# Kernel tuning notes

Hardware: AMD Instinct MI355X
Metric: run time of the kernel (lower is better)

## Reference

```python
import jax, jax.numpy as jnp
import numpy as np

PC_RANGE = np.array([-20.0, -20.0, -2.3, 20.0, 20.0, 0.9], np.float32)
GRID = np.array([0.1, 0.1, 0.1], np.float32)
K = 5                      # kernel_size
C_IN, C_OUT = 128, 128
BS, G = 8, 2000
SPATIAL = tuple(int(s) for s in ((PC_RANGE[3:] - PC_RANGE[:3]) / GRID).astype(np.int32))  # (400,400,32)


def setup_inputs() -> dict:
    key = jax.random.key(0)
    k1, k2, k3 = jax.random.split(key, 3)
    instance_feature = jax.random.normal(k1, (BS, G, C_IN), jnp.float32)
    anchor = jax.random.uniform(k2, (BS, G, 3), jnp.float32)          # normalized xyz in [0,1)
    w = jax.random.normal(k3, (K ** 3, C_IN, C_OUT), jnp.float32) * 0.02  # SubMConv3d weight, flattened offsets
    return {"instance_feature": instance_feature, "anchor": anchor, "w": w}


def _voxel_indices(anchor):
    # cartesian(): map normalized anchor xyz into the pc_range box, then voxelize.
    lo = jnp.asarray(PC_RANGE[:3])
    hi = jnp.asarray(PC_RANGE[3:])
    xyz = anchor[..., :3] * (hi - lo) + lo                 # [bs, g, 3]
    idx = ((xyz - lo) / jnp.asarray(GRID)).astype(jnp.int32)
    return idx


def reference(instance_feature, anchor, w):
    bs, g, c = instance_feature.shape
    n = bs * g
    idx = _voxel_indices(anchor).reshape(n, 3)             # [n, 3] int32 voxel coords
    bidx = jnp.repeat(jnp.arange(bs, dtype=jnp.int32), g)  # [n]
    Dx, Dy, Dz = SPATIAL

    # Rulebook substitute: dense voxel -> point-id lookup (-1 = inactive).
    grid = jnp.full((bs, Dx, Dy, Dz), -1, jnp.int32)
    grid = grid.at[bidx, idx[:, 0], idx[:, 1], idx[:, 2]].set(jnp.arange(n, dtype=jnp.int32))

    feats = instance_feature.reshape(n, c)
    r = (K - 1) // 2
    ax = jnp.arange(-r, r + 1, dtype=jnp.int32)
    offs = jnp.stack(jnp.meshgrid(ax, ax, ax, indexing="ij"), -1).reshape(-1, 3)  # [K^3, 3]
    dims = jnp.asarray([Dx, Dy, Dz], jnp.int32)

    # Submanifold conv: gather neighbor features per kernel offset, matmul, accumulate.
    def step(acc, inp):
        off, wk = inp                                       # off [3], wk [Cin, Cout]
        nb = idx + off[None, :]                             # [n, 3]
        inb = jnp.all((nb >= 0) & (nb < dims[None, :]), axis=-1)
        nbc = jnp.clip(nb, 0, dims[None, :] - 1)
        j = grid[bidx, nbc[:, 0], nbc[:, 1], nbc[:, 2]]     # [n] neighbor point id or -1
        valid = inb & (j >= 0)
        fj = jnp.where(valid[:, None], feats[jnp.clip(j, 0, n - 1)], 0.0)  # [n, Cin]
        return acc + fj @ wk, None

    out0 = jnp.zeros((n, C_OUT), feats.dtype)
    out, _ = jax.lax.scan(step, out0, (offs, w))
    return out.reshape(bs, g, C_OUT)                        # output_proj = Identity
```

## Files before the change

kernel.cpp:

```cpp
#include <hip/hip_runtime.h>
#include <stdint.h>

#define BSZ 8
#define GQ 2000
#define NPTS (BSZ * GQ)
#define CH 128
#define TM 16
#define NTHR 256
#define AS_LD 129
#define KB 32
#define ZPAD 32
#define EMPTY16 0xAAAAu
#define BHCAP 64
#define HIT_CAP 8192

#define GCNT_OFF  83886080
#define GHITS_OFF (GCNT_OFF + 256)

__device__ __forceinline__ int3 voxel_idx(const float* __restrict__ anchor, int i,
                                          float sx, float sy, float sz,
                                          float lx, float ly, float lz, float g) {
    float ax = anchor[i * 3 + 0];
    float ay = anchor[i * 3 + 1];
    float az = anchor[i * 3 + 2];
    float x = __fadd_rn(__fmul_rn(ax, sx), lx);
    float y = __fadd_rn(__fmul_rn(ay, sy), ly);
    float z = __fadd_rn(__fmul_rn(az, sz), lz);
    int ix = (int)__fdiv_rn(__fsub_rn(x, lx), g);
    int iy = (int)__fdiv_rn(__fsub_rn(y, ly), g);
    int iz = (int)__fdiv_rn(__fsub_rn(z, lz), g);
    return make_int3(ix, iy, iz);
}

__global__ void build_grid_kernel(const float* __restrict__ anchor,
                                  unsigned int* __restrict__ grid32,
                                  int* __restrict__ gcnt,
                                  float sx, float sy, float sz,
                                  float lx, float ly, float lz, float g,
                                  int Dx, int Dy, int Dz) {
    int i = blockIdx.x * blockDim.x + threadIdx.x;
    if (i == 0) gcnt[0] = 0;
    if (i >= NPTS) return;
    int3 v = voxel_idx(anchor, i, sx, sy, sz, lx, ly, lz, g);
    if (v.x < 0 || v.x >= Dx || v.y < 0 || v.y >= Dy || v.z < 0 || v.z >= Dz) return;
    int b = i / GQ;
    size_t cell = ((size_t)(b * Dx + v.x) * Dy + v.y) * ZPAD + v.z;
    unsigned int* wp = grid32 + (cell >> 1);
    int sh = (int)(cell & 1) * 16;
    unsigned int old = *wp;
    for (;;) {
        unsigned int cur = (old >> sh) & 0xFFFFu;
        unsigned int nj = (cur == EMPTY16) ? (unsigned int)i
                          : (cur > (unsigned int)i ? cur : (unsigned int)i);
        unsigned int neu = (old & ~(0xFFFFu << sh)) | (nj << sh);
        unsigned int got = atomicCAS(wp, old, neu);
        if (got == old) break;
        old = got;
    }
}

__global__ void __launch_bounds__(NTHR)
fused_kernel(const float* __restrict__ feat,
             const float* __restrict__ anchor,
             const float* __restrict__ w,
             const unsigned short* __restrict__ grid16,
             int* __restrict__ gcnt,
             int2* __restrict__ ghits,
             float* __restrict__ out,
             float sx, float sy, float sz,
             float lx, float ly, float lz, float g,
             int Dx, int Dy, int Dz) {
    __shared__ float As[TM * AS_LD];
    __shared__ float Bs[KB * CH];
    __shared__ int4  vox[TM];
    __shared__ int   selfj[TM];
    __shared__ int   s_cnt;
    __shared__ int   s_base;
    __shared__ int   s_hits[BHCAP];

    int rowbase = blockIdx.x * TM;
    int t = threadIdx.x;

    if (t == 0) { s_cnt = 0; s_base = 0; }
    if (t < TM) {
        int i = rowbase + t;
        int3 v = voxel_idx(anchor, i, sx, sy, sz, lx, ly, lz, g);
        vox[t] = make_int4(v.x, v.y, v.z, i / GQ);
        selfj[t] = -1;
    }
    __syncthreads();

    #pragma unroll
    for (int it = 0; it < 2; ++it) {
        int f = t + it * NTHR;
        bool tvalid = f < TM * 25;
        int p = tvalid ? f / 25 : 0;
        int col = f - p * 25;
        int4 v = vox[p];
        int ox = col / 5 - 2;
        int oy = col - (col / 5) * 5 - 2;
        int nx = v.x + ox, ny = v.y + oy;
        int zlo = v.z - 2; if (zlo < 0) zlo = 0;
        int zhi = v.z + 2; if (zhi > Dz - 1) zhi = Dz - 1;
        bool colok = tvalid && nx >= 0 && nx < Dx && ny >= 0 && ny < Dy && zlo <= zhi;
        unsigned short ee[8];
        int zbase = (zlo >> 2) * 4;
        if (colok) {
            int g0 = zlo >> 2;
            int g1 = g0 + 1; if (g1 > (ZPAD / 4 - 1)) g1 = ZPAD / 4 - 1;
            size_t colbase = ((size_t)(v.w * Dx + nx) * Dy + ny) * ZPAD;
            ushort4 q0 = *(const ushort4*)(grid16 + colbase + g0 * 4);
            ushort4 q1 = *(const ushort4*)(grid16 + colbase + g1 * 4);
            ee[0] = q0.x; ee[1] = q0.y; ee[2] = q0.z; ee[3] = q0.w;
            ee[4] = q1.x; ee[5] = q1.y; ee[6] = q1.z; ee[7] = q1.w;
        } else {
            #pragma unroll
            for (int c = 0; c < 8; ++c) ee[c] = 0xFFFF;
        }
        #pragma unroll
        for (int c = 0; c < 8; ++c) {
            int z4 = zbase + c;
            if (!colok || z4 < zlo || z4 > zhi) continue;
            int j = ee[c];
            if (j >= NPTS) continue;
            int oz = z4 - v.z;
            int koff = (ox + 2) * 25 + (oy + 2) * 5 + (oz + 2);
            if (koff == 62) {
                selfj[p] = j;
            } else {
                int pos = atomicAdd(&s_cnt, 1);
                if (pos < BHCAP) s_hits[pos] = (p << 21) | (koff << 14) | j;
            }
        }
    }
    __syncthreads();

    int nh = s_cnt < BHCAP ? s_cnt : BHCAP;
    if (t == 0 && nh > 0) s_base = atomicAdd(gcnt, nh);
    __syncthreads();
    if (t < nh) {
        int e = s_hits[t];
        int p = e >> 21;
        int pos = s_base + t;
        if (pos < HIT_CAP)
            ghits[pos] = make_int2(((rowbase + p) << 7) | ((e >> 14) & 0x7F),
                                   e & 0x3FFF);
    }

    #pragma unroll
    for (int f = t; f < TM * 32; f += NTHR) {
        int r = f >> 5;
        int c4 = f & 31;
        int j = selfj[r];
        float4 val = make_float4(0.f, 0.f, 0.f, 0.f);
        if (j >= 0) val = *(const float4*)(feat + (size_t)j * CH + c4 * 4);
        float* dst = As + r * AS_LD + c4 * 4;
        dst[0] = val.x; dst[1] = val.y; dst[2] = val.z; dst[3] = val.w;
    }

    int tc = t & 31;
    int tr = t >> 5;
    int r0 = tr * 2;

    float acc[2][4];
    #pragma unroll
    for (int a = 0; a < 2; ++a)
        #pragma unroll
        for (int b = 0; b < 4; ++b) acc[a][b] = 0.f;

    const float* B = w + (size_t)62 * CH * CH;

    #pragma unroll
    for (int chunk = 0; chunk < CH / KB; ++chunk) {
        __syncthreads();
        #pragma unroll
        for (int f = t; f < KB * 32; f += NTHR) {
            int kk = f >> 5;
            int c4 = f & 31;
            *(float4*)(Bs + kk * CH + c4 * 4) =
                *(const float4*)(B + (size_t)(chunk * KB + kk) * CH + c4 * 4);
        }
        __syncthreads();

        #pragma unroll 4
        for (int kk = 0; kk < KB; ++kk) {
            float4 b4 = *(const float4*)(Bs + kk * CH + tc * 4);
            float a0 = As[(r0 + 0) * AS_LD + chunk * KB + kk];
            float a1 = As[(r0 + 1) * AS_LD + chunk * KB + kk];
            acc[0][0] = fmaf(a0, b4.x, acc[0][0]); acc[0][1] = fmaf(a0, b4.y, acc[0][1]);
            acc[0][2] = fmaf(a0, b4.z, acc[0][2]); acc[0][3] = fmaf(a0, b4.w, acc[0][3]);
            acc[1][0] = fmaf(a1, b4.x, acc[1][0]); acc[1][1] = fmaf(a1, b4.y, acc[1][1]);
            acc[1][2] = fmaf(a1, b4.z, acc[1][2]); acc[1][3] = fmaf(a1, b4.w, acc[1][3]);
        }
    }

    #pragma unroll
    for (int rr = 0; rr < 2; ++rr) {
        int i = rowbase + r0 + rr;
        float4 v = make_float4(acc[rr][0], acc[rr][1], acc[rr][2], acc[rr][3]);
        *(float4*)(out + (size_t)i * CH + tc * 4) = v;
    }
}

__global__ void __launch_bounds__(CH)
scatter_kernel(const float* __restrict__ feat,
               const float* __restrict__ w,
               const int2* __restrict__ ghits,
               const int* __restrict__ gcnt,
               float* __restrict__ out) {
    __shared__ float fbuf[CH];
    int n = gcnt[0];
    if (n > HIT_CAP) n = HIT_CAP;
    int t = threadIdx.x;
    for (int h = blockIdx.x; h < n; h += gridDim.x) {
        int2 e = ghits[h];
        int i = e.x >> 7;
        int k = e.x & 0x7F;
        int j = e.y;
        __syncthreads();
        fbuf[t] = feat[(size_t)j * CH + t];
        __syncthreads();
        const float* wk = w + (size_t)k * CH * CH + t;
        float a0 = 0.f, a1 = 0.f, a2 = 0.f, a3 = 0.f;
        #pragma unroll 16
        for (int c = 0; c < CH; c += 4) {
            a0 = fmaf(fbuf[c + 0], wk[(c + 0) * CH], a0);
            a1 = fmaf(fbuf[c + 1], wk[(c + 1) * CH], a1);
            a2 = fmaf(fbuf[c + 2], wk[(c + 2) * CH], a2);
            a3 = fmaf(fbuf[c + 3], wk[(c + 3) * CH], a3);
        }
        atomicAdd(&out[(size_t)i * CH + t], (a0 + a1) + (a2 + a3));
    }
}

extern "C" void kernel_launch(void* const* d_in, const int* in_sizes, int n_in,
                              void* d_out, int out_size, void* d_ws, size_t ws_size,
                              hipStream_t stream) {
    const float* feat   = (const float*)d_in[0];
    const float* anchor = (const float*)d_in[1];
    const float* w      = (const float*)d_in[2];
    float* out = (float*)d_out;

    char* ws = (char*)d_ws;
    unsigned int*   grid32 = (unsigned int*)ws;
    unsigned short* grid16 = (unsigned short*)ws;
    int*  gcnt  = (int*)(ws + GCNT_OFF);
    int2* ghits = (int2*)(ws + GHITS_OFF);

    float lx = -20.0f, ly = -20.0f, lz = -2.3f;
    float hx =  20.0f, hy =  20.0f, hz =  0.9f;
    float sx = hx - lx, sy = hy - ly, sz = hz - lz;
    float g = 0.1f;
    int Dx = (int)(sx / g);
    int Dy = (int)(sy / g);
    int Dz = (int)(sz / g);

    build_grid_kernel<<<(NPTS + 255) / 256, 256, 0, stream>>>(
        anchor, grid32, gcnt, sx, sy, sz, lx, ly, lz, g, Dx, Dy, Dz);

    fused_kernel<<<NPTS / TM, NTHR, 0, stream>>>(
        feat, anchor, w, grid16, gcnt, ghits, out,
        sx, sy, sz, lx, ly, lz, g, Dx, Dy, Dz);

    scatter_kernel<<<2048, CH, 0, stream>>>(feat, w, ghits, gcnt, out);
}
```

Measured before the change: 99.30 us.

## Fold neighbor-hit scatter into fused kernel and enlarge self-GEMM tile

Removes the separate scatter kernel and its global hit list and atomics. Each block now processes its own neighbor hits in batches of eight: it stages the neighbor features in shared memory, computes the per-offset matvec and adds the result into register accumulators. The dense self-offset GEMM also grows from 16 to 32 rows per block, with a transposed A tile so each thread reads a float4 and keeps a 4x4 register tile. This saves one launch and the global atomic traffic, at the cost of serialized per-block hit work and fewer blocks.

```diff
diff --git a/kernel.cpp b/kernel.cpp
--- a/kernel.cpp
+++ b/kernel.cpp
@@ -5,17 +5,15 @@
 #define GQ 2000
 #define NPTS (BSZ * GQ)
 #define CH 128
-#define TM 16
+#define TM 32
 #define NTHR 256
-#define AS_LD 129
+#define ASK_LD 36
 #define KB 32
 #define ZPAD 32
 #define EMPTY16 0xAAAAu
 #define BHCAP 64
-#define HIT_CAP 8192
-
-#define GCNT_OFF  83886080
-#define GHITS_OFF (GCNT_OFF + 256)
+#define HBATCH 8
+
 
 __device__ __forceinline__ int3 voxel_idx(const float* __restrict__ anchor, int i,
                                           float sx, float sy, float sz,
@@ -34,12 +32,10 @@
 
 __global__ void build_grid_kernel(const float* __restrict__ anchor,
                                   unsigned int* __restrict__ grid32,
-                                  int* __restrict__ gcnt,
                                   float sx, float sy, float sz,
                                   float lx, float ly, float lz, float g,
                                   int Dx, int Dy, int Dz) {
     int i = blockIdx.x * blockDim.x + threadIdx.x;
-    if (i == 0) gcnt[0] = 0;
     if (i >= NPTS) return;
     int3 v = voxel_idx(anchor, i, sx, sy, sz, lx, ly, lz, g);
     if (v.x < 0 || v.x >= Dx || v.y < 0 || v.y >= Dy || v.z < 0 || v.z >= Dz) return;
@@ -64,24 +60,21 @@
              const float* __restrict__ anchor,
              const float* __restrict__ w,
              const unsigned short* __restrict__ grid16,
-             int* __restrict__ gcnt,
-             int2* __restrict__ ghits,
              float* __restrict__ out,
              float sx, float sy, float sz,
              float lx, float ly, float lz, float g,
              int Dx, int Dy, int Dz) {
-    __shared__ float As[TM * AS_LD];
+    __shared__ float Ask[CH * ASK_LD];
     __shared__ float Bs[KB * CH];
     __shared__ int4  vox[TM];
     __shared__ int   selfj[TM];
     __shared__ int   s_cnt;
-    __shared__ int   s_base;
     __shared__ int   s_hits[BHCAP];
 
     int rowbase = blockIdx.x * TM;
     int t = threadIdx.x;
 
-    if (t == 0) { s_cnt = 0; s_base = 0; }
+    if (t == 0) s_cnt = 0;
     if (t < TM) {
         int i = rowbase + t;
         int3 v = voxel_idx(anchor, i, sx, sy, sz, lx, ly, lz, g);
@@ -91,7 +84,7 @@
     __syncthreads();
 
     #pragma unroll
-    for (int it = 0; it < 2; ++it) {
+    for (int it = 0; it < (TM * 25 + NTHR - 1) / NTHR; ++it) {
         int f = t + it * NTHR;
         bool tvalid = f < TM * 25;
         int p = tvalid ? f / 25 : 0;
@@ -135,36 +128,26 @@
     }
     __syncthreads();
 
-    int nh = s_cnt < BHCAP ? s_cnt : BHCAP;
-    if (t == 0 && nh > 0) s_base = atomicAdd(gcnt, nh);
-    __syncthreads();
-    if (t < nh) {
-        int e = s_hits[t];
-        int p = e >> 21;
-        int pos = s_base + t;
-        if (pos < HIT_CAP)
-            ghits[pos] = make_int2(((rowbase + p) << 7) | ((e >> 14) & 0x7F),
-                                   e & 0x3FFF);
-    }
-
-    #pragma unroll
-    for (int f = t; f < TM * 32; f += NTHR) {
+    #pragma unroll
+    for (int f = t; f < TM * (CH / 4); f += NTHR) {
         int r = f >> 5;
         int c4 = f & 31;
         int j = selfj[r];
         float4 val = make_float4(0.f, 0.f, 0.f, 0.f);
         if (j >= 0) val = *(const float4*)(feat + (size_t)j * CH + c4 * 4);
-        float* dst = As + r * AS_LD + c4 * 4;
-        dst[0] = val.x; dst[1] = val.y; dst[2] = val.z; dst[3] = val.w;
+        Ask[(c4 * 4 + 0) * ASK_LD + r] = val.x;
+        Ask[(c4 * 4 + 1) * ASK_LD + r] = val.y;
+        Ask[(c4 * 4 + 2) * ASK_LD + r] = val.z;
+        Ask[(c4 * 4 + 3) * ASK_LD + r] = val.w;
     }
 
     int tc = t & 31;
     int tr = t >> 5;
-    int r0 = tr * 2;
-
-    float acc[2][4];
-    #pragma unroll
-    for (int a = 0; a < 2; ++a)
+    int r0 = tr * 4;
+
+    float acc[4][4];
+    #pragma unroll
+    for (int a = 0; a < 4; ++a)
         #pragma unroll
         for (int b = 0; b < 4; ++b) acc[a][b] = 0.f;
 
@@ -182,54 +165,81 @@
         }
         __syncthreads();
 
-        #pragma unroll 4
+        #pragma unroll 8
         for (int kk = 0; kk < KB; ++kk) {
             float4 b4 = *(const float4*)(Bs + kk * CH + tc * 4);
-            float a0 = As[(r0 + 0) * AS_LD + chunk * KB + kk];
-            float a1 = As[(r0 + 1) * AS_LD + chunk * KB + kk];
-            acc[0][0] = fmaf(a0, b4.x, acc[0][0]); acc[0][1] = fmaf(a0, b4.y, acc[0][1]);
-            acc[0][2] = fmaf(a0, b4.z, acc[0][2]); acc[0][3] = fmaf(a0, b4.w, acc[0][3]);
-            acc[1][0] = fmaf(a1, b4.x, acc[1][0]); acc[1][1] = fmaf(a1, b4.y, acc[1][1]);
-            acc[1][2] = fmaf(a1, b4.z, acc[1][2]); acc[1][3] = fmaf(a1, b4.w, acc[1][3]);
-        }
-    }
-
-    #pragma unroll
-    for (int rr = 0; rr < 2; ++rr) {
+            float4 a4 = *(const float4*)(Ask + (chunk * KB + kk) * ASK_LD + r0);
+            acc[0][0] = fmaf(a4.x, b4.x, acc[0][0]); acc[0][1] = fmaf(a4.x, b4.y, acc[0][1]);
+            acc[0][2] = fmaf(a4.x, b4.z, acc[0][2]); acc[0][3] = fmaf(a4.x, b4.w, acc[0][3]);
+            acc[1][0] = fmaf(a4.y, b4.x, acc[1][0]); acc[1][1] = fmaf(a4.y, b4.y, acc[1][1]);
+            acc[1][2] = fmaf(a4.y, b4.z, acc[1][2]); acc[1][3] = fmaf(a4.y, b4.w, acc[1][3]);
+            acc[2][0] = fmaf(a4.z, b4.x, acc[2][0]); acc[2][1] = fmaf(a4.z, b4.y, acc[2][1]);
+            acc[2][2] = fmaf(a4.z, b4.z, acc[2][2]); acc[2][3] = fmaf(a4.z, b4.w, acc[2][3]);
+            acc[3][0] = fmaf(a4.w, b4.x, acc[3][0]); acc[3][1] = fmaf(a4.w, b4.y, acc[3][1]);
+            acc[3][2] = fmaf(a4.w, b4.z, acc[3][2]); acc[3][3] = fmaf(a4.w, b4.w, acc[3][3]);
+        }
+    }
+
+    __syncthreads();
+    int nh = s_cnt < BHCAP ? s_cnt : BHCAP;
+    float* FB = Ask;
+    float* HO = Bs;
+    for (int base = 0; base < nh; base += HBATCH) {
+        int nb = nh - base; if (nb > HBATCH) nb = HBATCH;
+        #pragma unroll
+        for (int f = t; f < HBATCH * (CH / 4); f += NTHR) {
+            int s = f >> 5;
+            if (s < nb) {
+                int c4 = f & 31;
+                int j = s_hits[base + s] & 0x3FFF;
+                *(float4*)(FB + s * CH + c4 * 4) =
+                    *(const float4*)(feat + (size_t)j * CH + c4 * 4);
+            }
+        }
+        __syncthreads();
+        if (tr < nb) {
+            int e = s_hits[base + tr];
+            int koff = (e >> 14) & 0x7F;
+            const float* wk = w + (size_t)koff * CH * CH + tc * 4;
+            float hx = 0.f, hy = 0.f, hz = 0.f, hw = 0.f;
+            #pragma unroll 16
+            for (int k = 0; k < CH; ++k) {
+                float a = FB[tr * CH + k];
+                float4 wv = *(const float4*)(wk + (size_t)k * CH);
+                hx = fmaf(a, wv.x, hx); hy = fmaf(a, wv.y, hy);
+                hz = fmaf(a, wv.z, hz); hw = fmaf(a, wv.w, hw);
+            }
+            HO[tr * CH + tc * 4 + 0] = hx;
+            HO[tr * CH + tc * 4 + 1] = hy;
+            HO[tr * CH + tc * 4 + 2] = hz;
+            HO[tr * CH + tc * 4 + 3] = hw;
+        }
+        __syncthreads();
+        for (int s = 0; s < nb; ++s) {
+            int e = s_hits[base + s];
+            int p = e >> 21;
+            if ((p >> 2) == tr) {
+                int pr = p & 3;
+                float h0 = HO[s * CH + tc * 4 + 0];
+                float h1 = HO[s * CH + tc * 4 + 1];
+                float h2 = HO[s * CH + tc * 4 + 2];
+                float h3 = HO[s * CH + tc * 4 + 3];
+                #pragma unroll
+                for (int rr = 0; rr < 4; ++rr)
+                    if (rr == pr) {
+                        acc[rr][0] += h0; acc[rr][1] += h1;
+                        acc[rr][2] += h2; acc[rr][3] += h3;
+                    }
+            }
+        }
+        __syncthreads();
+    }
+
+    #pragma unroll
+    for (int rr = 0; rr < 4; ++rr) {
         int i = rowbase + r0 + rr;
         float4 v = make_float4(acc[rr][0], acc[rr][1], acc[rr][2], acc[rr][3]);
         *(float4*)(out + (size_t)i * CH + tc * 4) = v;
-    }
-}
-
-__global__ void __launch_bounds__(CH)
-scatter_kernel(const float* __restrict__ feat,
-               const float* __restrict__ w,
-               const int2* __restrict__ ghits,
-               const int* __restrict__ gcnt,
-               float* __restrict__ out) {
-    __shared__ float fbuf[CH];
-    int n = gcnt[0];
-    if (n > HIT_CAP) n = HIT_CAP;
-    int t = threadIdx.x;
-    for (int h = blockIdx.x; h < n; h += gridDim.x) {
-        int2 e = ghits[h];
-        int i = e.x >> 7;
-        int k = e.x & 0x7F;
-        int j = e.y;
-        __syncthreads();
-        fbuf[t] = feat[(size_t)j * CH + t];
-        __syncthreads();
-        const float* wk = w + (size_t)k * CH * CH + t;
-        float a0 = 0.f, a1 = 0.f, a2 = 0.f, a3 = 0.f;
-        #pragma unroll 16
-        for (int c = 0; c < CH; c += 4) {
-            a0 = fmaf(fbuf[c + 0], wk[(c + 0) * CH], a0);
-            a1 = fmaf(fbuf[c + 1], wk[(c + 1) * CH], a1);
-            a2 = fmaf(fbuf[c + 2], wk[(c + 2) * CH], a2);
-            a3 = fmaf(fbuf[c + 3], wk[(c + 3) * CH], a3);
-        }
-        atomicAdd(&out[(size_t)i * CH + t], (a0 + a1) + (a2 + a3));
     }
 }
 
@@ -241,11 +251,8 @@
     const float* w      = (const float*)d_in[2];
     float* out = (float*)d_out;
 
-    char* ws = (char*)d_ws;
-    unsigned int*   grid32 = (unsigned int*)ws;
-    unsigned short* grid16 = (unsigned short*)ws;
-    int*  gcnt  = (int*)(ws + GCNT_OFF);
-    int2* ghits = (int2*)(ws + GHITS_OFF);
+    unsigned int*   grid32 = (unsigned int*)d_ws;
+    const unsigned short* grid16 = (const unsigned short*)d_ws;
 
     float lx = -20.0f, ly = -20.0f, lz = -2.3f;
     float hx =  20.0f, hy =  20.0f, hz =  0.9f;
@@ -256,11 +263,9 @@
     int Dz = (int)(sz / g);
 
     build_grid_kernel<<<(NPTS + 255) / 256, 256, 0, stream>>>(
-        anchor, grid32, gcnt, sx, sy, sz, lx, ly, lz, g, Dx, Dy, Dz);
+        anchor, grid32, sx, sy, sz, lx, ly, lz, g, Dx, Dy, Dz);
 
     fused_kernel<<<NPTS / TM, NTHR, 0, stream>>>(
-        feat, anchor, w, grid16, gcnt, ghits, out,
+        feat, anchor, w, grid16, out,
         sx, sy, sz, lx, ly, lz, g, Dx, Dy, Dz);
-
-    scatter_kernel<<<2048, CH, 0, stream>>>(feat, w, ghits, gcnt, out);
-}
+}
```

Measured after the change: 94.12 us. 5.2% less time.
